# Performance work log

Hardware: AMD Instinct MI355X
Metric: run time of the kernel (lower is better)

## Reference

```python
import jax, jax.numpy as jnp
import numpy as np


def setup_inputs() -> dict:
    key = jax.random.key(0)
    k1, k2 = jax.random.split(key)
    N, C, H, W = 8, 3, 512, 1024
    img = jax.random.normal(k1, (N, C, H, W), dtype=jnp.float32)
    flo = jax.random.normal(k2, (N, 2, H, W), dtype=jnp.float32)
    return {"img": img, "flo": flo}


def _splat(img_nhwc, ix, iy, w, H, W):
    # img_nhwc: (N,H,W,C); ix,iy: int32 (N,H,W) absolute target coords; w: (N,H,W)
    N = img_nhwc.shape[0]
    C = img_nhwc.shape[-1]
    valid = (ix >= 0) & (ix < H) & (iy >= 0) & (iy < W)
    w = jnp.where(valid, w, 0.0)
    ixc = jnp.clip(ix, 0, H - 1)
    iyc = jnp.clip(iy, 0, W - 1)
    n_idx = jnp.arange(N, dtype=jnp.int32)[:, None, None]
    tid = (n_idx * H + ixc) * W + iyc            # (N,H,W) flat index into N*H*W
    tid = tid.reshape(-1)
    vals = (img_nhwc * w[..., None]).reshape(-1, C)
    imgw = jnp.zeros((N * H * W, C), dtype=img_nhwc.dtype).at[tid].add(vals)
    onew = jnp.zeros((N * H * W,), dtype=img_nhwc.dtype).at[tid].add(w.reshape(-1))
    imgw = imgw.reshape(N, H, W, C).transpose(0, 3, 1, 2)          # (N,C,H,W)
    onew = jnp.broadcast_to(onew.reshape(N, 1, H, W), (N, C, H, W))
    return imgw, onew


def _forward(img, flo):
    N, C, H, W = img.shape
    y = flo[:, 0]                                # (N,H,W) row offset
    x = flo[:, 1]                                # (N,H,W) col offset
    x1 = jnp.floor(x); x2 = x1 + 1.0
    y1 = jnp.floor(y); y2 = y1 + 1.0
    # gaussian splat weights
    dx1 = (x - x1) ** 2; dx2 = (x - x2) ** 2
    dy1 = (y - y1) ** 2; dy2 = (y - y2) ** 2
    w11 = jnp.exp(-(dx1 + dy1)); w12 = jnp.exp(-(dx1 + dy2))
    w21 = jnp.exp(-(dx2 + dy1)); w22 = jnp.exp(-(dx2 + dy2))
    # base grid + integer shift -> absolute target coords
    bx = jnp.arange(H, dtype=jnp.int32)[None, :, None]   # row index
    by = jnp.arange(W, dtype=jnp.int32)[None, None, :]   # col index
    img_nhwc = img.transpose(0, 2, 3, 1)
    out = []
    for sx, sy, w in ((x1, y1, w11), (x1, y2, w12), (x2, y1, w21), (x2, y2, w22)):
        ix = sx.astype(jnp.int32) + bx
        iy = sy.astype(jnp.int32) + by
        out.append(_splat(img_nhwc, ix, iy, w, H, W))
    imgw = out[0][0] + out[1][0] + out[2][0] + out[3][0]
    o = out[0][1] + out[1][1] + out[2][1] + out[3][1]
    return imgw, o


def reference(img, flo):
    return _forward(img, flo)
```

## Files before the change

kernel.cpp:

```cpp
#include <hip/hip_runtime.h>
#include <stdint.h>

constexpr int Nn = 8;
constexpr int Cc = 3;
constexpr int Hh = 512;
constexpr int Ww = 1024;
constexpr int HW = Hh * Ww;
constexpr int NCHW = Nn * Cc * HW;

constexpr int TH = 16;
constexpr int TW = 32;
constexpr int R  = 4;
constexpr int RH = TH + 2 * R;
constexpr int RW = TW + 2 * R;
constexpr int NPIX = RH * RW;
constexpr int ITERS = (NPIX + 255) / 256;
constexpr int TILE_PIX = TH * TW;
constexpr int NP = (TH + 1) * (TW + 1);
constexpr int SLOTS = 5;

typedef float fvec4 __attribute__((ext_vector_type(4)));
typedef __attribute__((address_space(3))) float lds_f;

__device__ __forceinline__ void ds_fadd4(lds_f* p, float a, float b, float c, float d) {
    asm volatile(
        "ds_add_f32 %0, %1\n\t"
        "ds_add_f32 %0, %2 offset:2048\n\t"
        "ds_add_f32 %0, %3 offset:4096\n\t"
        "ds_add_f32 %0, %4 offset:6144"
        :: "v"(p), "v"(a), "v"(b), "v"(c), "v"(d) : "memory");
}

__global__ __launch_bounds__(256, 2) void splat_tiled(
        const float* __restrict__ img,
        const float* __restrict__ flo,
        float* __restrict__ out) {
    __shared__ unsigned int s_cnt[NP];
    __shared__ float s_slot[SLOTS * NP * 5];
    __shared__ float s_ovf[4 * TILE_PIX];
    const int tid = threadIdx.x;
    for (int i = tid; i < NP; i += 256) s_cnt[i] = 0u;
    {
        fvec4* a4 = (fvec4*)s_ovf;
        fvec4 z = {0.f, 0.f, 0.f, 0.f};
        a4[tid]       = z;
        a4[tid + 256] = z;
    }
    __syncthreads();

    const int tw0 = blockIdx.x * TW;
    const int th0 = blockIdx.y * TH;
    const int n   = blockIdx.z;
    const float* __restrict__ floy = flo + (size_t)(n * 2 + 0) * HW;
    const float* __restrict__ flox = flo + (size_t)(n * 2 + 1) * HW;
    const float* __restrict__ imgn = img + (size_t)n * Cc * HW;

    float sy[ITERS], sx[ITERS], u0[ITERS], u1[ITERS], u2[ITERS];
    #pragma unroll
    for (int it = 0; it < ITERS; ++it) {
        int i  = tid + 256 * it;
        int ic = i < NPIX ? i : NPIX - 1;
        int rh = ic / RW;
        int rw = ic - rh * RW;
        int h  = th0 - R + rh;
        int w  = tw0 - R + rw;
        int hc = h < 0 ? 0 : (h > Hh - 1 ? Hh - 1 : h);
        int wc = w < 0 ? 0 : (w > Ww - 1 ? Ww - 1 : w);
        int hwc = hc * Ww + wc;
        sy[it] = floy[hwc];
        sx[it] = flox[hwc];
        u0[it] = imgn[hwc];
        u1[it] = imgn[HW + hwc];
        u2[it] = imgn[2 * HW + hwc];
    }

    #pragma unroll
    for (int it = 0; it < ITERS; ++it) {
        int i  = tid + 256 * it;
        int rh = i / RW;
        int rw = i - rh * RW;
        int h  = th0 - R + rh;
        int w  = tw0 - R + rw;
        bool live = (i < NPIX) & (h >= 0) & (h < Hh) & (w >= 0) & (w < Ww);

        float y = sy[it], x = sx[it];
        float x1f = floorf(x), y1f = floorf(y);
        float fx = x - x1f, fy = y - y1f;
        int ox = (int)x1f, oy = (int)y1f;
        bool patchok = (ox >= -R) & (ox <= R - 1) & (oy >= -R) & (oy <= R - 1);
        int ah = ox + rh - R;
        int aw = oy + rw - R;
        bool rec = live & patchok & (ah >= -1) & (ah <= TH - 1)
                                  & (aw >= -1) & (aw <= TW - 1);
        if (rec) {
            int aIdx = (ah + 1) * (TW + 1) + (aw + 1);
            unsigned int idx = atomicAdd(&s_cnt[aIdx], 1u);
            if (idx < (unsigned)SLOTS) {
                float* e = &s_slot[((int)idx * NP + aIdx) * 5];
                e[0] = u0[it];
                e[1] = u1[it];
                e[2] = u2[it];
                e[3] = fx;
                e[4] = fy;
            } else {
                float i0 = u0[it], i1 = u1[it], i2 = u2[it];
                #pragma unroll
                for (int a = 0; a < 2; ++a) {
                    #pragma unroll
                    for (int b = 0; b < 2; ++b) {
                        int t_h = ah + a, t_w = aw + b;
                        if ((unsigned)t_h < (unsigned)TH && (unsigned)t_w < (unsigned)TW) {
                            float dx = fx - (float)a, dy = fy - (float)b;
                            float wt = __expf(-(dx * dx + dy * dy));
                            ds_fadd4((lds_f*)s_ovf + (t_h * TW + t_w),
                                     i0 * wt, i1 * wt, i2 * wt, wt);
                        }
                    }
                }
            }
        }
    }
    __syncthreads();

    float* __restrict__ imgw  = out;
    float* __restrict__ o_out = out + NCHW;
    const size_t nb = (size_t)n * Cc * HW;
    #pragma unroll
    for (int itr = 0; itr < 2; ++itr) {
        int pix = tid + 256 * itr;
        int lh = pix >> 5, lw = pix & 31;
        float s0 = s_ovf[pix];
        float s1 = s_ovf[TILE_PIX + pix];
        float s2 = s_ovf[2 * TILE_PIX + pix];
        float s3 = s_ovf[3 * TILE_PIX + pix];
        #pragma unroll
        for (int a = 0; a < 2; ++a) {
            #pragma unroll
            for (int b = 0; b < 2; ++b) {
                int aIdx = (lh - a + 1) * (TW + 1) + (lw - b + 1);
                unsigned int k = s_cnt[aIdx];
                if (k > (unsigned)SLOTS) k = SLOTS;
                #pragma unroll
                for (int j = 0; j < SLOTS; ++j) {
                    if ((unsigned)j < k) {
                        const float* e = &s_slot[(j * NP + aIdx) * 5];
                        float e0 = e[0], e1 = e[1], e2 = e[2];
                        float dx = e[3] - (float)a, dy = e[4] - (float)b;
                        float wt = __expf(-(dx * dx + dy * dy));
                        s0 += e0 * wt;
                        s1 += e1 * wt;
                        s2 += e2 * wt;
                        s3 += wt;
                    }
                }
            }
        }
        size_t hw = (size_t)(th0 + lh) * Ww + (tw0 + lw);
        __builtin_nontemporal_store(s0, imgw + nb + hw);
        __builtin_nontemporal_store(s1, imgw + nb + HW + hw);
        __builtin_nontemporal_store(s2, imgw + nb + 2 * HW + hw);
        __builtin_nontemporal_store(s3, o_out + nb + hw);
        __builtin_nontemporal_store(s3, o_out + nb + HW + hw);
        __builtin_nontemporal_store(s3, o_out + nb + 2 * HW + hw);
    }
}

__global__ __launch_bounds__(256) void rescan_all(
        const float* __restrict__ img,
        const float* __restrict__ flo,
        float* __restrict__ out) {
    float* imgw  = out;
    float* o_out = out + NCHW;
    unsigned int j = blockIdx.x * blockDim.x + threadIdx.x;
    if (j >= (unsigned)(Nn * HW / 4)) return;
    int n   = j / (HW / 4);
    int q   = j - n * (HW / 4);
    int hw0 = q * 4;
    const fvec4 y4 = *(const fvec4*)&flo[(size_t)(n * 2 + 0) * HW + hw0];
    const fvec4 x4 = *(const fvec4*)&flo[(size_t)(n * 2 + 1) * HW + hw0];
    #pragma unroll
    for (int k = 0; k < 4; ++k) {
        float x = x4[k], y = y4[k];
        if (x >= -(float)R && x < (float)R && y >= -(float)R && y < (float)R) continue;
        int hw = hw0 + k;
        int h = hw >> 10;
        int w = hw & (Ww - 1);
        float x1f = floorf(x), y1f = floorf(y);
        float fx = x - x1f, fy = y - y1f;
        int bx = (int)x1f, by = (int)y1f;
        float i0 = img[(size_t)(n * Cc + 0) * HW + hw];
        float i1 = img[(size_t)(n * Cc + 1) * HW + hw];
        float i2 = img[(size_t)(n * Cc + 2) * HW + hw];
        const size_t nb = (size_t)n * Cc * HW;
        #pragma unroll
        for (int a = 0; a < 2; ++a) {
            #pragma unroll
            for (int b = 0; b < 2; ++b) {
                int ix = h + bx + a;
                int iy = w + by + b;
                if (ix < 0 || ix >= Hh || iy < 0 || iy >= Ww) continue;
                float dx = fx - (float)a, dy = fy - (float)b;
                float wt = __expf(-(dx * dx + dy * dy));
                int t = ix * Ww + iy;
                atomicAdd(&imgw[nb + t], i0 * wt);
                atomicAdd(&imgw[nb + HW + t], i1 * wt);
                atomicAdd(&imgw[nb + 2 * HW + t], i2 * wt);
                atomicAdd(&o_out[nb + t], wt);
                atomicAdd(&o_out[nb + HW + t], wt);
                atomicAdd(&o_out[nb + 2 * HW + t], wt);
            }
        }
    }
}

extern "C" void kernel_launch(void* const* d_in, const int* in_sizes, int n_in,
                              void* d_out, int out_size, void* d_ws, size_t ws_size,
                              hipStream_t stream) {
    const float* img = (const float*)d_in[0];
    const float* flo = (const float*)d_in[1];
    float* out = (float*)d_out;
    (void)d_ws; (void)ws_size;

    dim3 block(256);
    dim3 grid(Ww / TW, Hh / TH, Nn);
    splat_tiled<<<grid, block, 0, stream>>>(img, flo, out);
    rescan_all<<<(Nn * HW / 4 + 255) / 256, 256, 0, stream>>>(img, flo, out);
}
```

Baseline: 229.0 us.

## Use tag-claimed primary slots with packed overflow buckets to shrink LDS footprint

Each splat anchor cell now has one primary payload slot, claimed by a tag-write race followed by a sync, instead of an atomic counter per cell. A small 3-slot overflow area with 8-bit packed atomic counters backs it, and records are packed as float4 with the fractional offsets quantized to 16 bits each. The smaller LDS footprint allows 3 blocks per CU instead of 2, and the block index is remapped so the batch index varies fastest. The change adds an extra barrier and introduces small quantization error in the splat weights.

After: 209.0 us. 1.1x faster.

```diff
diff --git a/kernel.cpp b/kernel.cpp
--- a/kernel.cpp
+++ b/kernel.cpp
@@ -16,8 +16,9 @@
 constexpr int NPIX = RH * RW;
 constexpr int ITERS = (NPIX + 255) / 256;
 constexpr int TILE_PIX = TH * TW;
-constexpr int NP = (TH + 1) * (TW + 1);
-constexpr int SLOTS = 5;
+constexpr int AWP = TW + 1;
+constexpr int NP  = (TH + 1) * AWP;
+constexpr int OVF_SLOTS = 3;
 
 typedef float fvec4 __attribute__((ext_vector_type(4)));
 typedef __attribute__((address_space(3))) float lds_f;
@@ -31,26 +32,31 @@
         :: "v"(p), "v"(a), "v"(b), "v"(c), "v"(d) : "memory");
 }
 
-__global__ __launch_bounds__(256, 2) void splat_tiled(
+__global__ __launch_bounds__(256, 3) void splat_tiled(
         const float* __restrict__ img,
         const float* __restrict__ flo,
         float* __restrict__ out) {
-    __shared__ unsigned int s_cnt[NP];
-    __shared__ float s_slot[SLOTS * NP * 5];
-    __shared__ float s_ovf[4 * TILE_PIX];
+    __shared__ unsigned int s_tag[NP];
+    __shared__ unsigned int s_ocnt[(NP + 3) / 4];
+    __shared__ alignas(16) float s_pay[NP * 4];
+    __shared__ alignas(16) float s_ovf[OVF_SLOTS * NP * 4];
+    __shared__ float s_pl[4 * TILE_PIX];
     const int tid = threadIdx.x;
-    for (int i = tid; i < NP; i += 256) s_cnt[i] = 0u;
+    for (int i = tid; i < NP; i += 256) s_tag[i] = 0u;
+    for (int i = tid; i < (NP + 3) / 4; i += 256) s_ocnt[i] = 0u;
     {
-        fvec4* a4 = (fvec4*)s_ovf;
+        fvec4* a4 = (fvec4*)s_pl;
         fvec4 z = {0.f, 0.f, 0.f, 0.f};
-        a4[tid]       = z;
+        a4[tid] = z;
         a4[tid + 256] = z;
     }
     __syncthreads();
 
-    const int tw0 = blockIdx.x * TW;
-    const int th0 = blockIdx.y * TH;
-    const int n   = blockIdx.z;
+    const int lin = blockIdx.x + 32 * blockIdx.y + 1024 * blockIdx.z;
+    const int n   = lin & 7;
+    const int t   = lin >> 3;
+    const int tw0 = (t & 31) * TW;
+    const int th0 = (t >> 5) * TH;
     const float* __restrict__ floy = flo + (size_t)(n * 2 + 0) * HW;
     const float* __restrict__ flox = flo + (size_t)(n * 2 + 1) * HW;
     const float* __restrict__ imgn = img + (size_t)n * Cc * HW;
@@ -74,6 +80,8 @@
         u2[it] = imgn[2 * HW + hwc];
     }
 
+    int aA[ITERS];
+    unsigned int tg[ITERS], fxy[ITERS];
     #pragma unroll
     for (int it = 0; it < ITERS; ++it) {
         int i  = tid + 256 * it;
@@ -92,28 +100,45 @@
         int aw = oy + rw - R;
         bool rec = live & patchok & (ah >= -1) & (ah <= TH - 1)
                                   & (aw >= -1) & (aw <= TW - 1);
-        if (rec) {
-            int aIdx = (ah + 1) * (TW + 1) + (aw + 1);
-            unsigned int idx = atomicAdd(&s_cnt[aIdx], 1u);
-            if (idx < (unsigned)SLOTS) {
-                float* e = &s_slot[((int)idx * NP + aIdx) * 5];
-                e[0] = u0[it];
-                e[1] = u1[it];
-                e[2] = u2[it];
-                e[3] = fx;
-                e[4] = fy;
+        int aIdx = (ah + 1) * AWP + (aw + 1);
+        tg[it]  = 0x80000000u | ((unsigned)(ox + 4) << 24) | ((unsigned)(oy + 4) << 16);
+        fxy[it] = (unsigned)(fx * 65535.0f + 0.5f)
+                | ((unsigned)(fy * 65535.0f + 0.5f) << 16);
+        aA[it]  = rec ? aIdx : -1;
+        if (rec) s_tag[aIdx] = tg[it];
+    }
+    __syncthreads();
+
+    #pragma unroll
+    for (int it = 0; it < ITERS; ++it) {
+        int a = aA[it];
+        if (a >= 0) {
+            if (s_tag[a] == tg[it]) {
+                fvec4 e = {u0[it], u1[it], u2[it], __uint_as_float(fxy[it])};
+                *(fvec4*)&s_pay[a * 4] = e;
             } else {
-                float i0 = u0[it], i1 = u1[it], i2 = u2[it];
-                #pragma unroll
-                for (int a = 0; a < 2; ++a) {
+                unsigned sh  = 8u * (unsigned)(a & 3);
+                unsigned old = atomicAdd(&s_ocnt[a >> 2], 1u << sh);
+                unsigned idx = (old >> sh) & 0xFFu;
+                if (idx < (unsigned)OVF_SLOTS) {
+                    fvec4 e = {u0[it], u1[it], u2[it], __uint_as_float(fxy[it])};
+                    *(fvec4*)&s_ovf[((int)idx * NP + a) * 4] = e;
+                } else {
+                    int ah = a / AWP - 1;
+                    int aw = a - (ah + 1) * AWP - 1;
+                    float fx = (float)(fxy[it] & 0xFFFFu) * (1.0f / 65535.0f);
+                    float fy = (float)(fxy[it] >> 16) * (1.0f / 65535.0f);
                     #pragma unroll
-                    for (int b = 0; b < 2; ++b) {
-                        int t_h = ah + a, t_w = aw + b;
-                        if ((unsigned)t_h < (unsigned)TH && (unsigned)t_w < (unsigned)TW) {
-                            float dx = fx - (float)a, dy = fy - (float)b;
-                            float wt = __expf(-(dx * dx + dy * dy));
-                            ds_fadd4((lds_f*)s_ovf + (t_h * TW + t_w),
-                                     i0 * wt, i1 * wt, i2 * wt, wt);
+                    for (int ca = 0; ca < 2; ++ca) {
+                        #pragma unroll
+                        for (int cb = 0; cb < 2; ++cb) {
+                            int t_h = ah + ca, t_w = aw + cb;
+                            if ((unsigned)t_h < (unsigned)TH && (unsigned)t_w < (unsigned)TW) {
+                                float dx = fx - (float)ca, dy = fy - (float)cb;
+                                float wt = __expf(-(dx * dx + dy * dy));
+                                ds_fadd4((lds_f*)s_pl + (t_h * TW + t_w),
+                                         u0[it] * wt, u1[it] * wt, u2[it] * wt, wt);
+                            }
                         }
                     }
                 }
@@ -125,32 +150,42 @@
     float* __restrict__ imgw  = out;
     float* __restrict__ o_out = out + NCHW;
     const size_t nb = (size_t)n * Cc * HW;
+    const fvec4* pay4 = (const fvec4*)s_pay;
+    const fvec4* ovf4 = (const fvec4*)s_ovf;
     #pragma unroll
     for (int itr = 0; itr < 2; ++itr) {
         int pix = tid + 256 * itr;
         int lh = pix >> 5, lw = pix & 31;
-        float s0 = s_ovf[pix];
-        float s1 = s_ovf[TILE_PIX + pix];
-        float s2 = s_ovf[2 * TILE_PIX + pix];
-        float s3 = s_ovf[3 * TILE_PIX + pix];
+        float s0 = s_pl[pix];
+        float s1 = s_pl[TILE_PIX + pix];
+        float s2 = s_pl[2 * TILE_PIX + pix];
+        float s3 = s_pl[3 * TILE_PIX + pix];
         #pragma unroll
         for (int a = 0; a < 2; ++a) {
             #pragma unroll
             for (int b = 0; b < 2; ++b) {
-                int aIdx = (lh - a + 1) * (TW + 1) + (lw - b + 1);
-                unsigned int k = s_cnt[aIdx];
-                if (k > (unsigned)SLOTS) k = SLOTS;
+                int ai = (lh - a + 1) * AWP + (lw - b + 1);
+                unsigned tgv = s_tag[ai];
+                if (tgv & 0x80000000u) {
+                    fvec4 e = pay4[ai];
+                    unsigned p = __float_as_uint(e[3]);
+                    float fx = (float)(p & 0xFFFFu) * (1.0f / 65535.0f);
+                    float fy = (float)(p >> 16) * (1.0f / 65535.0f);
+                    float dx = fx - (float)a, dy = fy - (float)b;
+                    float wt = __expf(-(dx * dx + dy * dy));
+                    s0 += e[0] * wt; s1 += e[1] * wt; s2 += e[2] * wt; s3 += wt;
+                }
+                unsigned k = (s_ocnt[ai >> 2] >> (8u * (unsigned)(ai & 3))) & 0xFFu;
                 #pragma unroll
-                for (int j = 0; j < SLOTS; ++j) {
-                    if ((unsigned)j < k) {
-                        const float* e = &s_slot[(j * NP + aIdx) * 5];
-                        float e0 = e[0], e1 = e[1], e2 = e[2];
-                        float dx = e[3] - (float)a, dy = e[4] - (float)b;
+                for (int j = 0; j < OVF_SLOTS; ++j) {
+                    if (j < (int)k) {
+                        fvec4 e = ovf4[j * NP + ai];
+                        unsigned p = __float_as_uint(e[3]);
+                        float fx = (float)(p & 0xFFFFu) * (1.0f / 65535.0f);
+                        float fy = (float)(p >> 16) * (1.0f / 65535.0f);
+                        float dx = fx - (float)a, dy = fy - (float)b;
                         float wt = __expf(-(dx * dx + dy * dy));
-                        s0 += e0 * wt;
-                        s1 += e1 * wt;
-                        s2 += e2 * wt;
-                        s3 += wt;
+                        s0 += e[0] * wt; s1 += e[1] * wt; s2 += e[2] * wt; s3 += wt;
                     }
                 }
             }
@@ -222,7 +257,7 @@
     (void)d_ws; (void)ws_size;
 
     dim3 block(256);
-    dim3 grid(Ww / TW, Hh / TH, Nn);
+    dim3 grid(32, 32, 8);
     splat_tiled<<<grid, block, 0, stream>>>(img, flo, out);
     rescan_all<<<(Nn * HW / 4 + 255) / 256, 256, 0, stream>>>(img, flo, out);
 }
```
